# Kernel tuning notes

Hardware: AMD Instinct MI355X
Metric: run time of the kernel (lower is better)

## Reference

```python
import jax, jax.numpy as jnp
import numpy as np

N = 100000   # nodes
E = 1600000  # edges
G = 512      # graphs
L = 3        # num_unit LEConv layers
D = 64       # hidden dim


def setup_inputs() -> dict:
    key = jax.random.key(0)
    ks = jax.random.split(key, 12)
    s = 1.0 / np.sqrt(D)
    x = jax.random.normal(ks[0], (N, 4), jnp.float32)
    edge_index = jax.random.randint(ks[1], (2, E), 0, N, dtype=jnp.int64)
    edge_attr = jax.random.uniform(ks[2], (E,), jnp.float32)
    batch = jnp.sort(jax.random.randint(ks[3], (N,), 0, G, dtype=jnp.int64))
    return {
        "x": x,
        "edge_index": edge_index,
        "edge_attr": edge_attr,
        "batch": batch,
        "W_emb": jax.random.normal(ks[4], (4, D), jnp.float32) * 0.5,
        "b_emb": jnp.zeros((D,), jnp.float32),
        "W1": jax.random.normal(ks[5], (L, D, D), jnp.float32) * s,  # LEConv lin1 (on x_j)
        "b1": jnp.zeros((L, D), jnp.float32),
        "W2": jax.random.normal(ks[6], (L, D, D), jnp.float32) * s,  # LEConv lin2 (on x_i, no bias)
        "W3": jax.random.normal(ks[7], (L, D, D), jnp.float32) * s,  # LEConv lin3 (root)
        "b3": jnp.zeros((L, D), jnp.float32),
        "Wl1": jax.random.normal(ks[8], (D, 32), jnp.float32) * s,
        "bl1": jnp.zeros((32,), jnp.float32),
        "Wl2": jax.random.normal(ks[9], (32, 3), jnp.float32) * (1.0 / np.sqrt(32)),
        "bl2": jnp.zeros((3,), jnp.float32),
    }


def reference(x, edge_index, edge_attr, batch, W_emb, b_emb,
              W1, b1, W2, W3, b3, Wl1, bl1, Wl2, bl2):
    src, dst = edge_index[0], edge_index[1]
    h = x @ W_emb + b_emb                          # [N, D]
    for l in range(L):
        a = h @ W1[l] + b1[l]                      # lin1(x) -> gathered at source j
        b = h @ W2[l]                              # lin2(x) -> gathered at target i
        # LEConv message: e_ij * (lin1(x_j) - lin2(x_i)), aggr='add' at target
        msg = edge_attr[:, None] * (a[src] - b[dst])   # [E, D]
        agg = jax.ops.segment_sum(msg, dst, num_segments=N)
        h = jax.nn.relu(agg + h @ W3[l] + b3[l])
    # global_mean_pool over graphs
    sums = jax.ops.segment_sum(h, batch, num_segments=G)              # [G, D]
    counts = jax.ops.segment_sum(jnp.ones((N,), h.dtype), batch, num_segments=G)
    graph_x = sums / jnp.maximum(counts, 1.0)[:, None]
    pred = jax.nn.relu(graph_x @ Wl1 + bl1) @ Wl2 + bl2               # [G, 3]
    return pred
```

## Files before the change

kernel.cpp:

```cpp
#include <hip/hip_runtime.h>
#include <hip/hip_bf16.h>

#define NNODES 100000
#define NEDGES 1600000
#define NGRAPH 512
#define DIM    64
#define NLAYER 3

#define NB   1000
#define BN   100
#define CAP  2048
#define SC_BLOCKS 256
#define EPB  6250
#define PACK_BLOCKS 18
#define ZERO_BLOCKS 2
#define NBLK 1563

typedef __attribute__((ext_vector_type(8))) short short8;
typedef __attribute__((ext_vector_type(4))) float float4v;
typedef unsigned long long u64;

__device__ __forceinline__ __hip_bfloat16 f2b(float f) { return __float2bfloat16(f); }
__device__ __forceinline__ unsigned short f2b_bits(float f) {
    __hip_bfloat16 h = __float2bfloat16(f);
    return *reinterpret_cast<unsigned short*>(&h);
}

__device__ __forceinline__ unsigned pack_rec(int src, unsigned wbits32) {
    unsigned w15 = ((wbits32 + 0x8000u) >> 16) & 0x7FFFu;
    return ((unsigned)src << 15) | w15;
}

#define ACC4(ACC, RR, VV) do {                                              \
    float _w = __uint_as_float(((RR) & 0x7FFFu) << 16);                     \
    unsigned _lo = (unsigned)(VV), _hi = (unsigned)((VV) >> 32);            \
    ACC[0] = fmaf(_w, __uint_as_float(_lo << 16), ACC[0]);                  \
    ACC[1] = fmaf(_w, __uint_as_float(_lo & 0xFFFF0000u), ACC[1]);          \
    ACC[2] = fmaf(_w, __uint_as_float(_hi << 16), ACC[2]);                  \
    ACC[3] = fmaf(_w, __uint_as_float(_hi & 0xFFFF0000u), ACC[3]);          \
} while (0)

__device__ __forceinline__ void gather_rounds(
    unsigned rec, int cnt, const u64* __restrict__ h64, int q, int p,
    float (&accA)[4], float (&accB)[4], float (&accC)[4], float (&accD)[4]) {
    int full = cnt >> 4;
    for (int t = 0; t < full; ++t) {
        int base = t * 16;
        unsigned rA = (unsigned)__shfl((int)rec, base + q, 64);
        unsigned rB = (unsigned)__shfl((int)rec, base + 4 + q, 64);
        unsigned rC = (unsigned)__shfl((int)rec, base + 8 + q, 64);
        unsigned rD = (unsigned)__shfl((int)rec, base + 12 + q, 64);
        u64 vA = h64[(size_t)(rA >> 15) * 16 + p];
        u64 vB = h64[(size_t)(rB >> 15) * 16 + p];
        u64 vC = h64[(size_t)(rC >> 15) * 16 + p];
        u64 vD = h64[(size_t)(rD >> 15) * 16 + p];
        ACC4(accA, rA, vA);
        ACC4(accB, rB, vB);
        ACC4(accC, rC, vC);
        ACC4(accD, rD, vD);
    }
    int rem = cnt & 15;
    if (rem) {
        int base = full << 4;
        unsigned rA = (unsigned)__shfl((int)rec, base + q, 64);
        u64 vA = h64[(size_t)(rA >> 15) * 16 + p];
        unsigned rB = 0u, rC = 0u, rD = 0u;
        u64 vB = 0, vC = 0, vD = 0;
        if (rem > 4) {
            rB = (unsigned)__shfl((int)rec, base + 4 + q, 64);
            vB = h64[(size_t)(rB >> 15) * 16 + p];
        }
        if (rem > 8) {
            rC = (unsigned)__shfl((int)rec, base + 8 + q, 64);
            vC = h64[(size_t)(rC >> 15) * 16 + p];
        }
        if (rem > 12) {
            rD = (unsigned)__shfl((int)rec, base + 12 + q, 64);
            vD = h64[(size_t)(rD >> 15) * 16 + p];
        }
        ACC4(accA, rA, vA);
        ACC4(accB, rB, vB);
        ACC4(accC, rC, vC);
        ACC4(accD, rD, vD);
    }
}


__global__ __launch_bounds__(256) void local_sort_kernel(
    const int* __restrict__ ei, const float* __restrict__ ea,
    int2* __restrict__ perm_raw, int2* __restrict__ offcnt,
    const float* __restrict__ W1, const float* __restrict__ W2,
    const float* __restrict__ W3, __hip_bfloat16* __restrict__ wpack,
    float* __restrict__ gsum) {
    int tid = threadIdx.x, k = blockIdx.x;
    if (k >= SC_BLOCKS + PACK_BLOCKS) {
        float4v z = {0.f, 0.f, 0.f, 0.f};
        int idx = (k - SC_BLOCKS - PACK_BLOCKS) * 256 + tid;
        for (int i = idx; i < NGRAPH * DIM / 4; i += ZERO_BLOCKS * 256)
            ((float4v*)gsum)[i] = z;
        return;
    }
    if (k >= SC_BLOCKS) {
        int unit = (k - SC_BLOCKS) * 4 + (tid >> 6);
        if (unit < NLAYER * 24) {
            int kh = unit & 1, tn = (unit >> 1) & 3, w = (unit >> 3) % 3, l = unit / 24;
            const float* Wsrc = (w == 0 ? W1 : (w == 1 ? W2 : W3)) + l * 4096;
            int L = tid & 63;
            __hip_bfloat16* dst = wpack + (size_t)unit * 512 + L * 8;
            int kb = 32 * kh + (L >> 4) * 8;
            int nb = 16 * tn + (L & 15);
            #pragma unroll
            for (int j = 0; j < 8; ++j)
                dst[j] = f2b(Wsrc[(kb + j) * 64 + nb]);
        }
        return;
    }
    __shared__ int cnt[NB];
    __shared__ int off[NB];
    __shared__ int partial[256];
    __shared__ int2 srec[EPB];
    int e0 = k * EPB;
    for (int i = tid; i < NB; i += 256) cnt[i] = 0;
    __syncthreads();
    for (int i = tid; i < EPB; i += 256)
        atomicAdd(&cnt[ei[NEDGES + e0 + i] / BN], 1);
    __syncthreads();
    int loc[4]; int s = 0;
    #pragma unroll
    for (int j = 0; j < 4; ++j) {
        int b = tid * 4 + j;
        int v = (b < NB) ? cnt[b] : 0;
        loc[j] = s; s += v;
    }
    partial[tid] = s;
    __syncthreads();
    for (int o = 1; o < 256; o <<= 1) {
        int t = (tid >= o) ? partial[tid - o] : 0;
        __syncthreads();
        partial[tid] += t;
        __syncthreads();
    }
    int excl = partial[tid] - s;
    #pragma unroll
    for (int j = 0; j < 4; ++j) {
        int b = tid * 4 + j;
        if (b < NB) off[b] = excl + loc[j];
    }
    __syncthreads();
    for (int b = tid; b < NB; b += 256)
        offcnt[(size_t)k * NB + b] = make_int2(off[b], cnt[b]);
    __syncthreads();
    for (int i = tid; i < EPB; i += 256) {
        int e = e0 + i;
        int src = ei[e];
        int d = ei[NEDGES + e];
        float w = ea[e];
        int bin = d / BN;
        int dloc = d - bin * BN;
        int pos = atomicAdd(&off[bin], 1);
        srec[pos] = make_int2(src | (dloc << 20), __float_as_int(w));
    }
    __syncthreads();
    for (int i = tid; i < EPB; i += 256)
        perm_raw[e0 + i] = srec[i];
}

__global__ __launch_bounds__(256) void bucket_csr_kernel(
    const int2* __restrict__ perm_raw, const int2* __restrict__ offcnt,
    unsigned* __restrict__ perm2, int2* __restrict__ rows, float* __restrict__ wdeg) {
    __shared__ int2     recs[CAP];
    __shared__ unsigned recs2u[CAP];
    __shared__ int   pscan[256];
    __shared__ int   sprefix[SC_BLOCKS + 1];
    __shared__ int   boff[SC_BLOCKS];
    __shared__ int   cnt[BN];
    __shared__ int   start[BN];
    __shared__ int   cur[BN];
    __shared__ float ws[BN];
    int b = blockIdx.x, tid = threadIdx.x;
    if (tid < BN) { cnt[tid] = 0; ws[tid] = 0.f; }
    int2 oc = offcnt[(size_t)tid * NB + b];
    boff[tid] = oc.x;
    int c = oc.y;
    pscan[tid] = c;
    __syncthreads();
    for (int o = 1; o < 256; o <<= 1) {
        int t = (tid >= o) ? pscan[tid - o] : 0;
        __syncthreads();
        pscan[tid] += t;
        __syncthreads();
    }
    sprefix[tid] = pscan[tid] - c;
    if (tid == 255) sprefix[256] = pscan[255];
    __syncthreads();
    int n = min(sprefix[SC_BLOCKS], CAP);
    for (int i = tid; i < n; i += 256) {
        int lo = 0, hi = SC_BLOCKS;
        while (hi - lo > 1) { int m = (lo + hi) >> 1; if (sprefix[m] <= i) lo = m; else hi = m; }
        int2 rec = perm_raw[lo * EPB + boff[lo] + (i - sprefix[lo])];
        recs[i] = rec;
        atomicAdd(&cnt[rec.x >> 20], 1);
        atomicAdd(&ws[rec.x >> 20], __int_as_float(rec.y));
    }
    __syncthreads();
    {
        int v = (tid < BN) ? cnt[tid] : 0;
        pscan[tid] = v;
        __syncthreads();
        for (int o = 1; o < 128; o <<= 1) {
            int t = (tid >= o) ? pscan[tid - o] : 0;
            __syncthreads();
            pscan[tid] += t;
            __syncthreads();
        }
        if (tid < BN) start[tid] = pscan[tid] - v;
    }
    __syncthreads();
    if (tid < BN) {
        cur[tid] = start[tid];
        int base = b * CAP + start[tid];
        rows[b * BN + tid] = make_int2(base, base + cnt[tid]);
        wdeg[b * BN + tid] = ws[tid];
    }
    __syncthreads();
    for (int i = tid; i < n; i += 256) {
        int2 rec = recs[i];
        int pos = atomicAdd(&cur[rec.x >> 20], 1);
        recs2u[pos] = pack_rec(rec.x & 0xFFFFF, (unsigned)rec.y);
    }
    __syncthreads();
    for (int i = tid; i < n; i += 256)
        perm2[(size_t)b * CAP + i] = recs2u[i];
}


__global__ __launch_bounds__(256) void embed_kernel(
    const float* __restrict__ x, const float* __restrict__ Wemb,
    const float* __restrict__ bemb, __hip_bfloat16* __restrict__ h) {
    int t = blockIdx.x * 256 + threadIdx.x;
    int node = t >> 4, d0 = (t & 15) * 4;
    if (node >= NNODES) return;
    float4v xv = *(const float4v*)&x[(size_t)node * 4];
    u64 w0 = 0;
    #pragma unroll
    for (int j = 0; j < 4; ++j) {
        int ch = d0 + j;
        float s = bemb[ch];
        #pragma unroll
        for (int k = 0; k < 4; ++k) s = fmaf(xv[k], Wemb[k * 64 + ch], s);
        w0 |= (u64)f2b_bits(s) << (16 * j);
    }
    ((u64*)h)[(size_t)node * 16 + (t & 15)] = w0;
}


template <int LAST>
__global__ __launch_bounds__(256) void layer_kernel(
    const __hip_bfloat16* __restrict__ hin, __hip_bfloat16* __restrict__ hout,
    const int2* __restrict__ rows, const unsigned* __restrict__ perm2,
    const float* __restrict__ wdeg, const __hip_bfloat16* __restrict__ wpack,
    const float* __restrict__ b1, const float* __restrict__ b3,
    const int* __restrict__ batch, float* __restrict__ gsum) {
    __shared__ __align__(16) unsigned char mbytes[4 * 2048];
    int tid = threadIdx.x;
    int lane = tid & 63, wv = tid >> 6;
    int q = lane >> 4, p = lane & 15;
    int m0w = blockIdx.x * 64 + wv * 16;
    const u64* h64 = (const u64*)hin;

    int2 rall = rows[min(m0w + p, NNODES - 1)];
    int st_n = __shfl(rall.x, 0, 64);
    int en_n = __shfl(rall.y, 0, 64);
    if (m0w >= NNODES) en_n = st_n;
    unsigned rec_n = (lane < min(en_n - st_n, 64)) ? perm2[st_n + lane] : 0u;

    for (int nl = 0; nl < 16; ++nl) {
        int st = st_n, en = en_n;
        unsigned rec = rec_n;
        if (nl < 15) {
            st_n = __shfl(rall.x, nl + 1, 64);
            en_n = __shfl(rall.y, nl + 1, 64);
            if (m0w + nl + 1 >= NNODES) en_n = st_n;
            rec_n = (lane < min(en_n - st_n, 64)) ? perm2[st_n + lane] : 0u;
        }
        float accA[4] = {0.f, 0.f, 0.f, 0.f};
        float accB[4] = {0.f, 0.f, 0.f, 0.f};
        float accC[4] = {0.f, 0.f, 0.f, 0.f};
        float accD[4] = {0.f, 0.f, 0.f, 0.f};
        gather_rounds(rec, min(en - st, 64), h64, q, p, accA, accB, accC, accD);
        for (int cb = st + 64; cb < en; cb += 64) {
            unsigned rec2 = (lane < en - cb) ? perm2[cb + lane] : 0u;
            gather_rounds(rec2, min(en - cb, 64), h64, q, p, accA, accB, accC, accD);
        }
        #pragma unroll
        for (int j = 0; j < 4; ++j) accA[j] = (accA[j] + accB[j]) + (accC[j] + accD[j]);
        #pragma unroll
        for (int j = 0; j < 4; ++j) accA[j] += __shfl_xor(accA[j], 16, 64);
        #pragma unroll
        for (int j = 0; j < 4; ++j) accA[j] += __shfl_xor(accA[j], 32, 64);
        if (q == 0) {
            u64 w0 = (u64)f2b_bits(accA[0]) | ((u64)f2b_bits(accA[1]) << 16) |
                     ((u64)f2b_bits(accA[2]) << 32) | ((u64)f2b_bits(accA[3]) << 48);
            int off = (wv * 2048 + nl * 128 + p * 8) ^ ((nl & 7) << 4);
            *(u64*)(mbytes + off) = w0;
        }
    }

    float4v acc[3][4] = {};
    const short8* wp = (const short8*)wpack;
    int node_c = min(m0w + p, NNODES - 1);
    #pragma unroll
    for (int kh = 0; kh < 2; ++kh) {
        int roff = (wv * 2048 + p * 128 + kh * 64 + q * 16) ^ ((p & 7) << 4);
        short8 am = *(const short8*)(mbytes + roff);
        short8 ah = *(const short8*)((const short*)hin + (size_t)node_c * 64 + kh * 32 + q * 8);
        #pragma unroll
        for (int w = 0; w < 3; ++w) {
            #pragma unroll
            for (int tn = 0; tn < 4; ++tn) {
                short8 bfrag = wp[(size_t)((w * 4 + tn) * 2 + kh) * 64 + lane];
                acc[w][tn] = __builtin_amdgcn_mfma_f32_16x16x32_bf16(
                    w == 0 ? am : ah, bfrag, acc[w][tn], 0, 0, 0);
            }
        }
    }

    float b1v[4], b3v[4];
    #pragma unroll
    for (int tn = 0; tn < 4; ++tn) {
        b1v[tn] = b1[tn * 16 + p];
        b3v[tn] = b3[tn * 16 + p];
    }
    if (!LAST) {
        #pragma unroll
        for (int reg = 0; reg < 4; ++reg) {
            int node = m0w + q * 4 + reg;
            if (node < NNODES) {
                float wd = wdeg[node];
                #pragma unroll
                for (int tn = 0; tn < 4; ++tn) {
                    float s = acc[0][tn][reg] + acc[2][tn][reg] + b3v[tn] +
                              wd * (b1v[tn] - acc[1][tn][reg]);
                    hout[(size_t)node * 64 + tn * 16 + p] = f2b(fmaxf(s, 0.f));
                }
            }
        }
    } else {
        float val[4][4];
        int gb[4];
        #pragma unroll
        for (int reg = 0; reg < 4; ++reg) {
            int node = m0w + q * 4 + reg;
            int nc = min(node, NNODES - 1);
            float wd = wdeg[nc];
            gb[reg] = batch[nc];
            bool ok = node < NNODES;
            #pragma unroll
            for (int tn = 0; tn < 4; ++tn) {
                float s = acc[0][tn][reg] + acc[2][tn][reg] + b3v[tn] +
                          wd * (b1v[tn] - acc[1][tn][reg]);
                val[reg][tn] = ok ? fmaxf(s, 0.f) : 0.f;
            }
        }
        int glo = batch[min(m0w, NNODES - 1)];
        int ghi = batch[min(m0w + 15, NNODES - 1)];
        for (int g = glo; g <= ghi; ++g) {
            #pragma unroll
            for (int tn = 0; tn < 4; ++tn) {
                float part = 0.f;
                #pragma unroll
                for (int reg = 0; reg < 4; ++reg)
                    part += (gb[reg] == g) ? val[reg][tn] : 0.f;
                part += __shfl_xor(part, 16, 64);
                part += __shfl_xor(part, 32, 64);
                if (q == 0) atomicAdd(&gsum[g * 64 + tn * 16 + p], part);
            }
        }
    }
}


__global__ __launch_bounds__(64) void mlp_kernel(
    const float* __restrict__ gsum, const int* __restrict__ batch,
    const float* __restrict__ Wl1, const float* __restrict__ bl1,
    const float* __restrict__ Wl2, const float* __restrict__ bl2,
    float* __restrict__ out) {
    __shared__ int lohi[2];
    __shared__ float gxl[64];
    __shared__ float hid[32];
    int g = blockIdx.x, t = threadIdx.x;
    if (t < 2) {
        int target = g + t;
        int lo = 0, hi = NNODES;
        while (lo < hi) { int m = (lo + hi) >> 1; if (batch[m] < target) lo = m + 1; else hi = m; }
        lohi[t] = lo;
    }
    __syncthreads();
    int cnt = lohi[1] - lohi[0];
    gxl[t] = gsum[g * 64 + t] / (float)max(cnt, 1);
    __syncthreads();
    if (t < 32) {
        float s = bl1[t];
        for (int k = 0; k < 64; ++k) s = fmaf(gxl[k], Wl1[k * 32 + t], s);
        hid[t] = fmaxf(s, 0.f);
    }
    __syncthreads();
    if (t < 3) {
        float s = bl2[t];
        for (int k = 0; k < 32; ++k) s = fmaf(hid[k], Wl2[k * 3 + t], s);
        out[g * 3 + t] = s;
    }
}


extern "C" void kernel_launch(void* const* d_in, const int* in_sizes, int n_in,
                              void* d_out, int out_size, void* d_ws, size_t ws_size,
                              hipStream_t stream) {
    const float* x    = (const float*)d_in[0];
    const int*   ei   = (const int*)d_in[1];
    const float* ea   = (const float*)d_in[2];
    const int*   bat  = (const int*)d_in[3];
    const float* Wemb = (const float*)d_in[4];
    const float* bemb = (const float*)d_in[5];
    const float* W1   = (const float*)d_in[6];
    const float* b1   = (const float*)d_in[7];
    const float* W2   = (const float*)d_in[8];
    const float* W3   = (const float*)d_in[9];
    const float* b3   = (const float*)d_in[10];
    const float* Wl1  = (const float*)d_in[11];
    const float* bl1  = (const float*)d_in[12];
    const float* Wl2  = (const float*)d_in[13];
    const float* bl2  = (const float*)d_in[14];
    float* out = (float*)d_out;

    char* ws = (char*)d_ws;
    __hip_bfloat16*  h_b      = (__hip_bfloat16*) (ws + 0);
    __hip_bfloat16*  h_a      = (__hip_bfloat16*) (ws + 12800000);
    int2*            perm_raw = (int2*)           (ws + 25600000);
    unsigned*        perm2    = (unsigned*)       (ws + 38400000);
    int2*            rows     = (int2*)           (ws + 46592000);
    int2*            offcnt   = (int2*)           (ws + 47392000);
    float*           wdeg     = (float*)          (ws + 49440000);
    __hip_bfloat16*  wpack    = (__hip_bfloat16*) (ws + 49840000);
    float*           gsum     = (float*)          (ws + 49913728);

    local_sort_kernel<<<SC_BLOCKS + PACK_BLOCKS + ZERO_BLOCKS, 256, 0, stream>>>(
        ei, ea, perm_raw, offcnt, W1, W2, W3, wpack, gsum);
    bucket_csr_kernel<<<NB, 256, 0, stream>>>(perm_raw, offcnt, perm2, rows, wdeg);
    embed_kernel<<<(NNODES * 16 + 255) / 256, 256, 0, stream>>>(x, Wemb, bemb, h_a);

    layer_kernel<0><<<NBLK, 256, 0, stream>>>(
        h_a, h_b, rows, perm2, wdeg, wpack, b1, b3, bat, gsum);
    layer_kernel<0><<<NBLK, 256, 0, stream>>>(
        h_b, h_a, rows, perm2, wdeg, wpack + (size_t)24 * 512, b1 + 64, b3 + 64, bat, gsum);
    layer_kernel<1><<<NBLK, 256, 0, stream>>>(
        h_a, h_b, rows, perm2, wdeg, wpack + (size_t)48 * 512, b1 + 128, b3 + 128, bat, gsum);

    mlp_kernel<<<NGRAPH, 64, 0, stream>>>(gsum, bat, Wl1, bl1, Wl2, bl2, out);
}
```

Baseline: 288.7 us.

## Halve nodes per block in layer kernel and fuse embed into CSR kernel

Each layer block now covers 32 nodes instead of 64. Every wave gathers 8 nodes instead of 16, the results are exchanged through shared memory after a block barrier, and only two waves then run the MFMA transform. This gives twice as many blocks with shorter serial gather chains per wave, raising memory-level parallelism for the edge gathers, at the cost of idling half the waves during the matmul. The embedding kernel is merged into the CSR build kernel as extra blocks to save a launch, and bounds checks are dropped because 100000 divides evenly by 32. A launch-bounds occupancy hint of 8 is also added.

```diff
diff --git a/kernel.cpp b/kernel.cpp
--- a/kernel.cpp
+++ b/kernel.cpp
@@ -14,7 +14,8 @@
 #define EPB  6250
 #define PACK_BLOCKS 18
 #define ZERO_BLOCKS 2
-#define NBLK 1563
+#define NBLK32 3125
+#define EMB_BLOCKS 6250
 
 typedef __attribute__((ext_vector_type(8))) short short8;
 typedef __attribute__((ext_vector_type(4))) float float4v;
@@ -165,9 +166,11 @@
         perm_raw[e0 + i] = srec[i];
 }
 
-__global__ __launch_bounds__(256) void bucket_csr_kernel(
+__global__ __launch_bounds__(256) void csr_embed_kernel(
     const int2* __restrict__ perm_raw, const int2* __restrict__ offcnt,
-    unsigned* __restrict__ perm2, int2* __restrict__ rows, float* __restrict__ wdeg) {
+    unsigned* __restrict__ perm2, int2* __restrict__ rows, float* __restrict__ wdeg,
+    const float* __restrict__ x, const float* __restrict__ Wemb,
+    const float* __restrict__ bemb, __hip_bfloat16* __restrict__ h) {
     __shared__ int2     recs[CAP];
     __shared__ unsigned recs2u[CAP];
     __shared__ int   pscan[256];
@@ -178,6 +181,22 @@
     __shared__ int   cur[BN];
     __shared__ float ws[BN];
     int b = blockIdx.x, tid = threadIdx.x;
+    if (b >= NB) {
+        int t = (b - NB) * 256 + tid;
+        int node = t >> 4, d0 = (t & 15) * 4;
+        float4v xv = *(const float4v*)&x[(size_t)node * 4];
+        u64 w0 = 0;
+        #pragma unroll
+        for (int j = 0; j < 4; ++j) {
+            int ch = d0 + j;
+            float s = bemb[ch];
+            #pragma unroll
+            for (int k = 0; k < 4; ++k) s = fmaf(xv[k], Wemb[k * 64 + ch], s);
+            w0 |= (u64)f2b_bits(s) << (16 * j);
+        }
+        ((u64*)h)[(size_t)node * 16 + (t & 15)] = w0;
+        return;
+    }
     if (tid < BN) { cnt[tid] = 0; ws[tid] = 0.f; }
     int2 oc = offcnt[(size_t)tid * NB + b];
     boff[tid] = oc.x;
@@ -234,53 +253,31 @@
 }
 
 
-__global__ __launch_bounds__(256) void embed_kernel(
-    const float* __restrict__ x, const float* __restrict__ Wemb,
-    const float* __restrict__ bemb, __hip_bfloat16* __restrict__ h) {
-    int t = blockIdx.x * 256 + threadIdx.x;
-    int node = t >> 4, d0 = (t & 15) * 4;
-    if (node >= NNODES) return;
-    float4v xv = *(const float4v*)&x[(size_t)node * 4];
-    u64 w0 = 0;
-    #pragma unroll
-    for (int j = 0; j < 4; ++j) {
-        int ch = d0 + j;
-        float s = bemb[ch];
-        #pragma unroll
-        for (int k = 0; k < 4; ++k) s = fmaf(xv[k], Wemb[k * 64 + ch], s);
-        w0 |= (u64)f2b_bits(s) << (16 * j);
-    }
-    ((u64*)h)[(size_t)node * 16 + (t & 15)] = w0;
-}
-
-
 template <int LAST>
-__global__ __launch_bounds__(256) void layer_kernel(
+__global__ __launch_bounds__(256, 8) void layer_kernel(
     const __hip_bfloat16* __restrict__ hin, __hip_bfloat16* __restrict__ hout,
     const int2* __restrict__ rows, const unsigned* __restrict__ perm2,
     const float* __restrict__ wdeg, const __hip_bfloat16* __restrict__ wpack,
     const float* __restrict__ b1, const float* __restrict__ b3,
     const int* __restrict__ batch, float* __restrict__ gsum) {
-    __shared__ __align__(16) unsigned char mbytes[4 * 2048];
+    __shared__ __align__(16) unsigned char mbytes[32 * 128];
     int tid = threadIdx.x;
     int lane = tid & 63, wv = tid >> 6;
     int q = lane >> 4, p = lane & 15;
-    int m0w = blockIdx.x * 64 + wv * 16;
+    int m0 = blockIdx.x * 32 + wv * 8;
     const u64* h64 = (const u64*)hin;
 
-    int2 rall = rows[min(m0w + p, NNODES - 1)];
-    int st_n = __shfl(rall.x, 0, 64);
-    int en_n = __shfl(rall.y, 0, 64);
-    if (m0w >= NNODES) en_n = st_n;
+    int2 rl = rows[m0 + (lane & 7)];
+    int st_n = __shfl(rl.x, 0, 64);
+    int en_n = __shfl(rl.y, 0, 64);
     unsigned rec_n = (lane < min(en_n - st_n, 64)) ? perm2[st_n + lane] : 0u;
 
-    for (int nl = 0; nl < 16; ++nl) {
+    for (int nl = 0; nl < 8; ++nl) {
         int st = st_n, en = en_n;
         unsigned rec = rec_n;
-        if (nl < 15) {
-            st_n = __shfl(rall.x, nl + 1, 64);
-            en_n = __shfl(rall.y, nl + 1, 64);
-            if (m0w + nl + 1 >= NNODES) en_n = st_n;
+        if (nl < 7) {
+            st_n = __shfl(rl.x, nl + 1, 64);
+            en_n = __shfl(rl.y, nl + 1, 64);
             rec_n = (lane < min(en_n - st_n, 64)) ? perm2[st_n + lane] : 0u;
         }
         float accA[4] = {0.f, 0.f, 0.f, 0.f};
@@ -301,17 +298,21 @@
         if (q == 0) {
             u64 w0 = (u64)f2b_bits(accA[0]) | ((u64)f2b_bits(accA[1]) << 16) |
                      ((u64)f2b_bits(accA[2]) << 32) | ((u64)f2b_bits(accA[3]) << 48);
-            int off = (wv * 2048 + nl * 128 + p * 8) ^ ((nl & 7) << 4);
+            int row = wv * 8 + nl;
+            int off = (row * 128 + p * 8) ^ ((row & 7) << 4);
             *(u64*)(mbytes + off) = w0;
         }
     }
+    __syncthreads();
+    if (wv >= 2) return;
 
     float4v acc[3][4] = {};
     const short8* wp = (const short8*)wpack;
-    int node_c = min(m0w + p, NNODES - 1);
+    int row = wv * 16 + p;
+    int node_c = blockIdx.x * 32 + row;
     #pragma unroll
     for (int kh = 0; kh < 2; ++kh) {
-        int roff = (wv * 2048 + p * 128 + kh * 64 + q * 16) ^ ((p & 7) << 4);
+        int roff = (row * 128 + kh * 64 + q * 16) ^ ((row & 7) << 4);
         short8 am = *(const short8*)(mbytes + roff);
         short8 ah = *(const short8*)((const short*)hin + (size_t)node_c * 64 + kh * 32 + q * 8);
         #pragma unroll
@@ -331,18 +332,17 @@
         b1v[tn] = b1[tn * 16 + p];
         b3v[tn] = b3[tn * 16 + p];
     }
+    int tb = blockIdx.x * 32 + wv * 16;
     if (!LAST) {
         #pragma unroll
         for (int reg = 0; reg < 4; ++reg) {
-            int node = m0w + q * 4 + reg;
-            if (node < NNODES) {
-                float wd = wdeg[node];
-                #pragma unroll
-                for (int tn = 0; tn < 4; ++tn) {
-                    float s = acc[0][tn][reg] + acc[2][tn][reg] + b3v[tn] +
-                              wd * (b1v[tn] - acc[1][tn][reg]);
-                    hout[(size_t)node * 64 + tn * 16 + p] = f2b(fmaxf(s, 0.f));
-                }
+            int node = tb + q * 4 + reg;
+            float wd = wdeg[node];
+            #pragma unroll
+            for (int tn = 0; tn < 4; ++tn) {
+                float s = acc[0][tn][reg] + acc[2][tn][reg] + b3v[tn] +
+                          wd * (b1v[tn] - acc[1][tn][reg]);
+                hout[(size_t)node * 64 + tn * 16 + p] = f2b(fmaxf(s, 0.f));
             }
         }
     } else {
@@ -350,20 +350,18 @@
         int gb[4];
         #pragma unroll
         for (int reg = 0; reg < 4; ++reg) {
-            int node = m0w + q * 4 + reg;
-            int nc = min(node, NNODES - 1);
-            float wd = wdeg[nc];
-            gb[reg] = batch[nc];
-            bool ok = node < NNODES;
+            int node = tb + q * 4 + reg;
+            float wd = wdeg[node];
+            gb[reg] = batch[node];
             #pragma unroll
             for (int tn = 0; tn < 4; ++tn) {
                 float s = acc[0][tn][reg] + acc[2][tn][reg] + b3v[tn] +
                           wd * (b1v[tn] - acc[1][tn][reg]);
-                val[reg][tn] = ok ? fmaxf(s, 0.f) : 0.f;
+                val[reg][tn] = fmaxf(s, 0.f);
             }
         }
-        int glo = batch[min(m0w, NNODES - 1)];
-        int ghi = batch[min(m0w + 15, NNODES - 1)];
+        int glo = batch[tb];
+        int ghi = batch[tb + 15];
         for (int g = glo; g <= ghi; ++g) {
             #pragma unroll
             for (int tn = 0; tn < 4; ++tn) {
@@ -446,14 +444,14 @@
 
     local_sort_kernel<<<SC_BLOCKS + PACK_BLOCKS + ZERO_BLOCKS, 256, 0, stream>>>(
         ei, ea, perm_raw, offcnt, W1, W2, W3, wpack, gsum);
-    bucket_csr_kernel<<<NB, 256, 0, stream>>>(perm_raw, offcnt, perm2, rows, wdeg);
-    embed_kernel<<<(NNODES * 16 + 255) / 256, 256, 0, stream>>>(x, Wemb, bemb, h_a);
-
-    layer_kernel<0><<<NBLK, 256, 0, stream>>>(
+    csr_embed_kernel<<<NB + EMB_BLOCKS, 256, 0, stream>>>(
+        perm_raw, offcnt, perm2, rows, wdeg, x, Wemb, bemb, h_a);
+
+    layer_kernel<0><<<NBLK32, 256, 0, stream>>>(
         h_a, h_b, rows, perm2, wdeg, wpack, b1, b3, bat, gsum);
-    layer_kernel<0><<<NBLK, 256, 0, stream>>>(
+    layer_kernel<0><<<NBLK32, 256, 0, stream>>>(
         h_b, h_a, rows, perm2, wdeg, wpack + (size_t)24 * 512, b1 + 64, b3 + 64, bat, gsum);
-    layer_kernel<1><<<NBLK, 256, 0, stream>>>(
+    layer_kernel<1><<<NBLK32, 256, 0, stream>>>(
         h_a, h_b, rows, perm2, wdeg, wpack + (size_t)48 * 512, b1 + 128, b3 + 128, bat, gsum);
 
     mlp_kernel<<<NGRAPH, 64, 0, stream>>>(gsum, bat, Wl1, bl1, Wl2, bl2, out);
```

New measurement: 268.2 us. 1.08x faster.
